# Optimization experiments

Measured on AMD Instinct MI355X. Metric: run time of the kernel, lower is better.

Reference implementation:

```python
import jax, jax.numpy as jnp
import numpy as np

N_NODES = 100000
N_EDGES = 1600000
D_IN = 128
D_HID = 128
D_OUT = 64
N_LAYERS = 3
BN_EPS = 1e-5


def _mlp_block(h, W1, b1, g, be, W2, b2):
    # PyG MLP([c_in, h, h]): Linear -> BatchNorm -> ReLU -> Linear (plain last)
    h = h @ W1 + b1                      # [N, h]
    mu = jnp.mean(h, axis=0)
    var = jnp.var(h, axis=0)             # biased var, BN training-mode stats
    h = (h - mu) * jax.lax.rsqrt(var + BN_EPS) * g + be
    h = jax.nn.relu(h)
    return h @ W2 + b2


def setup_inputs() -> dict:
    key = jax.random.key(0)
    ks = jax.random.split(key, 16)
    s_in = 1.0 / np.sqrt(D_IN)
    s_h = 1.0 / np.sqrt(D_HID)
    x = jax.random.normal(ks[0], (N_NODES, D_IN), dtype=jnp.float32)
    edge_index = jax.random.randint(ks[1], (2, N_EDGES), 0, N_NODES, dtype=jnp.int64)
    return {
        "x": x,
        "edge_index": edge_index,
        # stacked per-conv MLP params (all layers are 128->128->128)
        "W1": jax.random.normal(ks[2], (N_LAYERS, D_IN, D_HID), jnp.float32) * s_in,
        "b1": jnp.zeros((N_LAYERS, D_HID), jnp.float32),
        "g1": jnp.ones((N_LAYERS, D_HID), jnp.float32),
        "be1": jnp.zeros((N_LAYERS, D_HID), jnp.float32),
        "W2": jax.random.normal(ks[3], (N_LAYERS, D_HID, D_HID), jnp.float32) * s_h,
        "b2": jnp.zeros((N_LAYERS, D_HID), jnp.float32),
        # final MLP([h, h, out])
        "fW1": jax.random.normal(ks[4], (D_HID, D_HID), jnp.float32) * s_h,
        "fb1": jnp.zeros((D_HID,), jnp.float32),
        "fg1": jnp.ones((D_HID,), jnp.float32),
        "fbe1": jnp.zeros((D_HID,), jnp.float32),
        "fW2": jax.random.normal(ks[5], (D_HID, D_OUT), jnp.float32) * s_h,
        "fb2": jnp.zeros((D_OUT,), jnp.float32),
    }


def reference(x, edge_index, W1, b1, g1, be1, W2, b2, fW1, fb1, fg1, fbe1, fW2, fb2):
    src, dst = edge_index[0], edge_index[1]
    for l in range(N_LAYERS):
        # GINConv, eps=0: nn((1+eps)*x + sum_{j->i} x_j)
        aggr = jax.ops.segment_sum(x[src], dst, num_segments=N_NODES)  # [N, d]
        h = x + aggr
        x = jax.nn.relu(_mlp_block(h, W1[l], b1[l], g1[l], be1[l], W2[l], b2[l]))
    # final MLP (dropout=0.5 is identity in eval mode)
    return _mlp_block(x, fW1, fb1, fg1, fbe1, fW2, fb2)
```

## Files before the change

### kernel.cpp

```cpp
#include <hip/hip_runtime.h>

#define NN 100000
#define NE 1600000
#define DD 128
#define CAP 64
#define NGROUP 256

static __device__ __forceinline__ unsigned short f2b(float f) {
  unsigned int x = __float_as_uint(f);
  unsigned int r = x + 0x7fffu + ((x >> 16) & 1u);
  return (unsigned short)(r >> 16);
}
static __device__ __forceinline__ float b2f(unsigned short u) {
  return __uint_as_float(((unsigned int)u) << 16);
}

typedef __attribute__((ext_vector_type(8))) short short8;
typedef __attribute__((ext_vector_type(4))) float f32x4;

union V8 {
  uint4 u4;
  short8 s8;
  unsigned short us[8];
};

__global__ void detect_k(const int* __restrict__ ei, int* __restrict__ flag) {
  int v = ei[2 * threadIdx.x + 1];
  unsigned long long b = __ballot(v != 0);
  if (threadIdx.x == 0) *flag = (b == 0ull) ? 1 : 0;
}

__global__ __launch_bounds__(256) void cast_k(const float* __restrict__ x,
                                              unsigned short* __restrict__ x16) {
  size_t i = ((size_t)blockIdx.x * 256 + threadIdx.x) * 8;
  f32x4 a = *(const f32x4*)(x + i);
  f32x4 b = *(const f32x4*)(x + i + 4);
  V8 v;
#pragma unroll
  for (int j = 0; j < 4; ++j) {
    v.us[j] = f2b(a[j]);
    v.us[4 + j] = f2b(b[j]);
  }
  *(uint4*)(x16 + i) = v.u4;
}

__global__ __launch_bounds__(256) void pack_k(const int* __restrict__ ei,
                                              int* __restrict__ packed,
                                              int* __restrict__ cnt,
                                              const int* __restrict__ flag) {
  const int mode = *flag;
  const int gid = blockIdx.x * 256 + threadIdx.x;
  int s, d;
  if (mode) {
    s = ei[2 * (size_t)gid];
    d = ei[2 * ((size_t)NE + gid)];
  } else {
    s = ei[gid];
    d = ei[NE + gid];
  }
  packed[2 * gid] = s;
  packed[2 * gid + 1] = d;
  if (gid < NN) cnt[gid] = 0;
}

__global__ __launch_bounds__(256) void scatter_k(const long long* __restrict__ packed,
                                                 int* __restrict__ cnt,
                                                 int* __restrict__ csr) {
  const int r = blockIdx.x & 7;
  const int g = blockIdx.x >> 3;
  const int lo = r * (NN / 8), hi = lo + (NN / 8);
  for (int e = g * 256 + threadIdx.x; e < NE; e += NGROUP * 256) {
    long long sd = __builtin_nontemporal_load(&packed[e]);
    const int s = (int)(sd & 0xffffffffll);
    const int d = (int)(sd >> 32);
    if (d >= lo && d < hi) {
      int c = atomicAdd(&cnt[d], 1);
      if (c < CAP) csr[(size_t)d * CAP + c] = s;
    }
  }
}

__global__ __launch_bounds__(256) void wprep_k(const float* __restrict__ W1,
                                               const float* __restrict__ W2,
                                               const float* __restrict__ fW1,
                                               const float* __restrict__ fW2,
                                               unsigned short* __restrict__ wt) {
  int b = blockIdx.x;
  const float* src;
  int moff, N;
  if (b < 192) {
    int m = b >> 6;
    src = W1 + m * 16384;
    moff = m * 16384;
    N = 128;
    b &= 63;
  } else if (b < 384) {
    int m = (b - 192) >> 6;
    src = W2 + m * 16384;
    moff = (3 + m) * 16384;
    N = 128;
    b = (b - 192) & 63;
  } else if (b < 448) {
    src = fW1;
    moff = 6 * 16384;
    N = 128;
    b -= 384;
  } else {
    src = fW2;
    moff = 7 * 16384;
    N = 64;
    b -= 448;
  }
  int idx = b * 256 + threadIdx.x;
  int n = idx >> 7, k = idx & 127;
  if (n < N) wt[moff + idx] = f2b(src[(size_t)k * N + n]);
}

template <int AMODE, int NCOLS, int EPI, int STATS>
__global__ __launch_bounds__(256) void gemm_k(const unsigned short* __restrict__ Aptr,
                                              const unsigned short* __restrict__ wT,
                                              const float* __restrict__ bias,
                                              const float* __restrict__ bn_stats,
                                              const float* __restrict__ gamma,
                                              const float* __restrict__ beta,
                                              void* __restrict__ Cptr,
                                              float* __restrict__ stats_out,
                                              const int* __restrict__ cnt,
                                              const int* __restrict__ csr) {
  __shared__ unsigned short bT[NCOLS][136];
  __shared__ float biasS[NCOLS];
  __shared__ float scS[128];
  __shared__ float shS[128];
  __shared__ float sS[NCOLS];
  __shared__ float s2S[NCOLS];
  const int tid = threadIdx.x;

  for (int i = tid; i < NCOLS * 16; i += 256) {
    int n = i >> 4, k8 = (i & 15) << 3;
    *(uint4*)&bT[n][k8] = *(const uint4*)(wT + n * 128 + k8);
  }
  if (tid < NCOLS) biasS[tid] = bias[tid];
  if (AMODE == 2 && tid < 128) {
    const float inv_n = 1.0f / (float)NN;
    float mu = bn_stats[tid] * inv_n;
    float var = bn_stats[128 + tid] * inv_n - mu * mu;
    float sc = gamma[tid] * rsqrtf(var + 1e-5f);
    scS[tid] = sc;
    shS[tid] = beta[tid] - mu * sc;
  }
  if (STATS && tid < NCOLS) {
    sS[tid] = 0.f;
    s2S[tid] = 0.f;
  }
  __syncthreads();

  const int wv = tid >> 6;
  const int lane = tid & 63;
  const int l16 = lane & 15;
  const int quad = lane >> 4;
  const int arow = blockIdx.x * 64 + wv * 16 + l16;
  const bool rv = arow < NN;

  V8 afs[4];
  if (AMODE == 3) {
    float ac[4][8];
#pragma unroll
    for (int kc = 0; kc < 4; ++kc) {
      V8 w;
      w.u4 = rv ? *(const uint4*)(Aptr + (size_t)arow * DD + kc * 32 + quad * 8)
                : make_uint4(0u, 0u, 0u, 0u);
#pragma unroll
      for (int j = 0; j < 8; ++j) ac[kc][j] = b2f(w.us[j]);
    }
    if (rv) {
      const size_t base = (size_t)arow * CAP;
      const int c = cnt[arow];
      int p = 0;
      for (; p + 2 <= c; p += 2) {
        const int s0 = csr[base + p], s1 = csr[base + p + 1];
        V8 w0[4], w1[4];
#pragma unroll
        for (int kc = 0; kc < 4; ++kc) {
          w0[kc].u4 = *(const uint4*)(Aptr + (size_t)s0 * DD + kc * 32 + quad * 8);
          w1[kc].u4 = *(const uint4*)(Aptr + (size_t)s1 * DD + kc * 32 + quad * 8);
        }
#pragma unroll
        for (int kc = 0; kc < 4; ++kc)
#pragma unroll
          for (int j = 0; j < 8; ++j)
            ac[kc][j] += b2f(w0[kc].us[j]) + b2f(w1[kc].us[j]);
      }
      if (p < c) {
        const int s0 = csr[base + p];
        V8 w0[4];
#pragma unroll
        for (int kc = 0; kc < 4; ++kc)
          w0[kc].u4 = *(const uint4*)(Aptr + (size_t)s0 * DD + kc * 32 + quad * 8);
#pragma unroll
        for (int kc = 0; kc < 4; ++kc)
#pragma unroll
          for (int j = 0; j < 8; ++j) ac[kc][j] += b2f(w0[kc].us[j]);
      }
    }
#pragma unroll
    for (int kc = 0; kc < 4; ++kc)
#pragma unroll
      for (int j = 0; j < 8; ++j) afs[kc].us[j] = f2b(ac[kc][j]);
  } else {
#pragma unroll
    for (int kc = 0; kc < 4; ++kc) {
      const int k0 = kc * 32 + quad * 8;
      afs[kc].u4 = rv ? *(const uint4*)(Aptr + (size_t)arow * DD + k0)
                      : make_uint4(0u, 0u, 0u, 0u);
      if (AMODE == 2) {
#pragma unroll
        for (int j = 0; j < 8; ++j) {
          float f = fmaf(b2f(afs[kc].us[j]), scS[k0 + j], shS[k0 + j]);
          afs[kc].us[j] = f2b(fmaxf(f, 0.0f));
        }
      }
    }
  }

  f32x4 acc[NCOLS / 16];
#pragma unroll
  for (int nt = 0; nt < NCOLS / 16; ++nt) acc[nt] = (f32x4)(0.0f);
#pragma unroll
  for (int kc = 0; kc < 4; ++kc) {
    const int k0 = kc * 32 + quad * 8;
#pragma unroll
    for (int nt = 0; nt < NCOLS / 16; ++nt) {
      V8 bf;
      bf.u4 = *(const uint4*)&bT[nt * 16 + l16][k0];
      acc[nt] = __builtin_amdgcn_mfma_f32_16x16x32_bf16(afs[kc].s8, bf.s8, acc[nt], 0, 0, 0);
    }
  }

  const int r0 = blockIdx.x * 64 + wv * 16 + quad * 4;
#pragma unroll
  for (int nt = 0; nt < NCOLS / 16; ++nt) {
    const int col = nt * 16 + l16;
    const float bv = biasS[col];
    float s = 0.f, s2 = 0.f;
#pragma unroll
    for (int i = 0; i < 4; ++i) {
      const int r = r0 + i;
      if (r < NN) {
        float v = acc[nt][i] + bv;
        if (EPI == 1) v = fmaxf(v, 0.0f);
        if (EPI == 2) {
          ((float*)Cptr)[(size_t)r * NCOLS + col] = v;
        } else {
          unsigned short us = f2b(v);
          ((unsigned short*)Cptr)[(size_t)r * NCOLS + col] = us;
          if (STATS) {
            float vr = b2f(us);
            s += vr;
            s2 += vr * vr;
          }
        }
      }
    }
    if (STATS) {
      s += __shfl_xor(s, 16);
      s += __shfl_xor(s, 32);
      s2 += __shfl_xor(s2, 16);
      s2 += __shfl_xor(s2, 32);
      if (quad == 0) {
        atomicAdd(&sS[col], s);
        atomicAdd(&s2S[col], s2);
      }
    }
  }
  if (STATS) {
    __syncthreads();
    if (tid < NCOLS) {
      atomicAdd(&stats_out[tid], sS[tid]);
      atomicAdd(&stats_out[128 + tid], s2S[tid]);
    }
  }
}

extern "C" void kernel_launch(void* const* d_in, const int* in_sizes, int n_in,
                              void* d_out, int out_size, void* d_ws, size_t ws_size,
                              hipStream_t stream) {
  const float* x = (const float*)d_in[0];
  const int* ei = (const int*)d_in[1];
  const float* W1 = (const float*)d_in[2];
  const float* b1 = (const float*)d_in[3];
  const float* g1 = (const float*)d_in[4];
  const float* be1 = (const float*)d_in[5];
  const float* W2 = (const float*)d_in[6];
  const float* b2 = (const float*)d_in[7];
  const float* fW1 = (const float*)d_in[8];
  const float* fb1 = (const float*)d_in[9];
  const float* fg1 = (const float*)d_in[10];
  const float* fbe1 = (const float*)d_in[11];
  const float* fW2 = (const float*)d_in[12];
  const float* fb2 = (const float*)d_in[13];

  char* ws = (char*)d_ws;
  unsigned short* x16 = (unsigned short*)ws;
  unsigned short* t16 = (unsigned short*)(ws + (size_t)25600000);
  int* packed = (int*)t16;
  int* csr = (int*)(ws + (size_t)51200000);
  int* cnt = (int*)(ws + (size_t)76800000);
  float* stats4 = (float*)(ws + (size_t)77200000);
  int* flag = (int*)(ws + (size_t)77204992);
  unsigned short* wt = (unsigned short*)(ws + (size_t)77210000);

  const int vecBlocks = (NN * DD) / (256 * 8);
  const int gemmBlocks = (NN + 63) / 64;
  const int edgeBlocks = NE / 256;
  const int filtBlocks = NGROUP * 8;

  detect_k<<<1, 64, 0, stream>>>(ei, flag);
  (void)hipMemsetAsync(stats4, 0, 4 * 256 * sizeof(float), stream);
  cast_k<<<vecBlocks, 256, 0, stream>>>(x, x16);
  pack_k<<<edgeBlocks, 256, 0, stream>>>(ei, packed, cnt, flag);
  wprep_k<<<480, 256, 0, stream>>>(W1, W2, fW1, fW2, wt);
  scatter_k<<<filtBlocks, 256, 0, stream>>>((const long long*)packed, cnt, csr);

  for (int l = 0; l < 3; ++l) {
    gemm_k<3, 128, 0, 1><<<gemmBlocks, 256, 0, stream>>>(
        x16, wt + (size_t)l * 16384, b1 + l * 128, nullptr, nullptr, nullptr, t16,
        stats4 + l * 256, cnt, csr);
    gemm_k<2, 128, 1, 0><<<gemmBlocks, 256, 0, stream>>>(
        t16, wt + (size_t)(3 + l) * 16384, b2 + l * 128, stats4 + l * 256,
        g1 + l * 128, be1 + l * 128, x16, nullptr, nullptr, nullptr);
  }

  gemm_k<1, 128, 0, 1><<<gemmBlocks, 256, 0, stream>>>(
      x16, wt + (size_t)6 * 16384, fb1, nullptr, nullptr, nullptr, t16,
      stats4 + 3 * 256, nullptr, nullptr);
  gemm_k<2, 64, 2, 0><<<gemmBlocks, 256, 0, stream>>>(
      t16, wt + (size_t)7 * 16384, fb2, stats4 + 3 * 256, fg1, fbe1, (float*)d_out,
      nullptr, nullptr, nullptr);
}
```

Before: 665.9 us.

## Split aggregation into column-chunked kernel with degree-sorted node order

Result: slower. 1.341 ms (+101.4%).

```diff
diff --git a/kernel.cpp b/kernel.cpp
--- a/kernel.cpp
+++ b/kernel.cpp
@@ -17,9 +17,11 @@
 
 typedef __attribute__((ext_vector_type(8))) short short8;
 typedef __attribute__((ext_vector_type(4))) float f32x4;
+typedef unsigned int v4u __attribute__((ext_vector_type(4)));
 
 union V8 {
   uint4 u4;
+  v4u v4;
   short8 s8;
   unsigned short us[8];
 };
@@ -31,17 +33,22 @@
 }
 
 __global__ __launch_bounds__(256) void cast_k(const float* __restrict__ x,
-                                              unsigned short* __restrict__ x16) {
-  size_t i = ((size_t)blockIdx.x * 256 + threadIdx.x) * 8;
-  f32x4 a = *(const f32x4*)(x + i);
-  f32x4 b = *(const f32x4*)(x + i + 4);
-  V8 v;
+                                              unsigned short* __restrict__ xc) {
+  const int g = blockIdx.y;
+  const int n = blockIdx.x * 256 + threadIdx.x;
+  if (n >= NN) return;
+  const float* xp = x + (size_t)n * DD + g * 16;
+  V8 o0, o1;
 #pragma unroll
   for (int j = 0; j < 4; ++j) {
-    v.us[j] = f2b(a[j]);
-    v.us[4 + j] = f2b(b[j]);
-  }
-  *(uint4*)(x16 + i) = v.u4;
+    o0.us[j] = f2b(xp[j]);
+    o0.us[4 + j] = f2b(xp[4 + j]);
+    o1.us[j] = f2b(xp[8 + j]);
+    o1.us[4 + j] = f2b(xp[12 + j]);
+  }
+  unsigned short* op = xc + ((size_t)g * NN + n) * 16;
+  *(uint4*)op = o0.u4;
+  *(uint4*)(op + 8) = o1.u4;
 }
 
 __global__ __launch_bounds__(256) void pack_k(const int* __restrict__ ei,
@@ -77,6 +84,38 @@
       int c = atomicAdd(&cnt[d], 1);
       if (c < CAP) csr[(size_t)d * CAP + c] = s;
     }
+  }
+}
+
+__global__ __launch_bounds__(256) void hist2_k(const int* __restrict__ cnt,
+                                               int* __restrict__ dbin) {
+  __shared__ int lb[CAP + 1];
+  if (threadIdx.x <= CAP) lb[threadIdx.x] = 0;
+  __syncthreads();
+  const int i = blockIdx.x * 256 + threadIdx.x;
+  if (i < NN) atomicAdd(&lb[min(cnt[i], CAP)], 1);
+  __syncthreads();
+  if (threadIdx.x <= CAP && lb[threadIdx.x]) atomicAdd(&dbin[threadIdx.x], lb[threadIdx.x]);
+}
+
+__global__ void dscan_k(const int* __restrict__ dbin, int* __restrict__ dcur) {
+  if (threadIdx.x == 0) {
+    int run = 0;
+    for (int i = 0; i <= CAP; ++i) {
+      dcur[i] = run;
+      run += dbin[i];
+    }
+  }
+}
+
+__global__ __launch_bounds__(256) void dorder_k(const int* __restrict__ cnt,
+                                                int* __restrict__ dcur,
+                                                int* __restrict__ order) {
+  const int i = blockIdx.x * 256 + threadIdx.x;
+  if (i < NN) {
+    int c = min(cnt[i], CAP);
+    int pos = atomicAdd(&dcur[c], 1);
+    order[pos] = i | (c << 24);
   }
 }
 
@@ -116,6 +155,64 @@
   if (n < N) wt[moff + idx] = f2b(src[(size_t)k * N + n]);
 }
 
+__global__ __launch_bounds__(256) void agg_k(const int* __restrict__ order,
+                                             const int* __restrict__ csr,
+                                             const unsigned short* __restrict__ xc,
+                                             unsigned short* __restrict__ hc) {
+  const int g = blockIdx.x & 7;
+  const unsigned short* xg = xc + (size_t)g * NN * 16;
+  unsigned short* hg = hc + (size_t)g * NN * 16;
+  const int stride = (gridDim.x >> 3) * 256;
+  for (int i = (blockIdx.x >> 3) * 256 + threadIdx.x; i < NN; i += stride) {
+    const int oc = order[i];
+    const int n = oc & 0xFFFFFF;
+    const int c = oc >> 24;
+    V8 v0, v1;
+    v0.u4 = *(const uint4*)(xg + (size_t)n * 16);
+    v1.u4 = *(const uint4*)(xg + (size_t)n * 16 + 8);
+    float acc[16];
+#pragma unroll
+    for (int j = 0; j < 8; ++j) {
+      acc[j] = b2f(v0.us[j]);
+      acc[8 + j] = b2f(v1.us[j]);
+    }
+    const int* row = csr + (size_t)n * CAP;
+    int p = 0;
+    for (; p + 2 <= c; p += 2) {
+      const int s0 = row[p], s1 = row[p + 1];
+      V8 a0, a1, b0, b1;
+      a0.u4 = *(const uint4*)(xg + (size_t)s0 * 16);
+      a1.u4 = *(const uint4*)(xg + (size_t)s0 * 16 + 8);
+      b0.u4 = *(const uint4*)(xg + (size_t)s1 * 16);
+      b1.u4 = *(const uint4*)(xg + (size_t)s1 * 16 + 8);
+#pragma unroll
+      for (int j = 0; j < 8; ++j) {
+        acc[j] += b2f(a0.us[j]) + b2f(b0.us[j]);
+        acc[8 + j] += b2f(a1.us[j]) + b2f(b1.us[j]);
+      }
+    }
+    if (p < c) {
+      const int s0 = row[p];
+      V8 a0, a1;
+      a0.u4 = *(const uint4*)(xg + (size_t)s0 * 16);
+      a1.u4 = *(const uint4*)(xg + (size_t)s0 * 16 + 8);
+#pragma unroll
+      for (int j = 0; j < 8; ++j) {
+        acc[j] += b2f(a0.us[j]);
+        acc[8 + j] += b2f(a1.us[j]);
+      }
+    }
+    V8 o0, o1;
+#pragma unroll
+    for (int j = 0; j < 8; ++j) {
+      o0.us[j] = f2b(acc[j]);
+      o1.us[j] = f2b(acc[8 + j]);
+    }
+    __builtin_nontemporal_store(o0.v4, (v4u*)(hg + (size_t)n * 16));
+    __builtin_nontemporal_store(o1.v4, (v4u*)(hg + (size_t)n * 16 + 8));
+  }
+}
+
 template <int AMODE, int NCOLS, int EPI, int STATS>
 __global__ __launch_bounds__(256) void gemm_k(const unsigned short* __restrict__ Aptr,
                                               const unsigned short* __restrict__ wT,
@@ -124,9 +221,7 @@
                                               const float* __restrict__ gamma,
                                               const float* __restrict__ beta,
                                               void* __restrict__ Cptr,
-                                              float* __restrict__ stats_out,
-                                              const int* __restrict__ cnt,
-                                              const int* __restrict__ csr) {
+                                              float* __restrict__ stats_out) {
   __shared__ unsigned short bT[NCOLS][136];
   __shared__ float biasS[NCOLS];
   __shared__ float scS[128];
@@ -162,62 +257,21 @@
   const bool rv = arow < NN;
 
   V8 afs[4];
-  if (AMODE == 3) {
-    float ac[4][8];
-#pragma unroll
-    for (int kc = 0; kc < 4; ++kc) {
-      V8 w;
-      w.u4 = rv ? *(const uint4*)(Aptr + (size_t)arow * DD + kc * 32 + quad * 8)
-                : make_uint4(0u, 0u, 0u, 0u);
-#pragma unroll
-      for (int j = 0; j < 8; ++j) ac[kc][j] = b2f(w.us[j]);
-    }
-    if (rv) {
-      const size_t base = (size_t)arow * CAP;
-      const int c = cnt[arow];
-      int p = 0;
-      for (; p + 2 <= c; p += 2) {
-        const int s0 = csr[base + p], s1 = csr[base + p + 1];
-        V8 w0[4], w1[4];
-#pragma unroll
-        for (int kc = 0; kc < 4; ++kc) {
-          w0[kc].u4 = *(const uint4*)(Aptr + (size_t)s0 * DD + kc * 32 + quad * 8);
-          w1[kc].u4 = *(const uint4*)(Aptr + (size_t)s1 * DD + kc * 32 + quad * 8);
-        }
-#pragma unroll
-        for (int kc = 0; kc < 4; ++kc)
-#pragma unroll
-          for (int j = 0; j < 8; ++j)
-            ac[kc][j] += b2f(w0[kc].us[j]) + b2f(w1[kc].us[j]);
-      }
-      if (p < c) {
-        const int s0 = csr[base + p];
-        V8 w0[4];
-#pragma unroll
-        for (int kc = 0; kc < 4; ++kc)
-          w0[kc].u4 = *(const uint4*)(Aptr + (size_t)s0 * DD + kc * 32 + quad * 8);
-#pragma unroll
-        for (int kc = 0; kc < 4; ++kc)
-#pragma unroll
-          for (int j = 0; j < 8; ++j) ac[kc][j] += b2f(w0[kc].us[j]);
-      }
-    }
-#pragma unroll
-    for (int kc = 0; kc < 4; ++kc)
-#pragma unroll
-      for (int j = 0; j < 8; ++j) afs[kc].us[j] = f2b(ac[kc][j]);
-  } else {
-#pragma unroll
-    for (int kc = 0; kc < 4; ++kc) {
+#pragma unroll
+  for (int kc = 0; kc < 4; ++kc) {
+    if (AMODE == 1) {
+      const int col8 = kc * 4 + quad;
+      const unsigned short* ap =
+          Aptr + ((size_t)(col8 >> 1) * NN + arow) * 16 + (col8 & 1) * 8;
+      afs[kc].u4 = rv ? *(const uint4*)ap : make_uint4(0u, 0u, 0u, 0u);
+    } else {
       const int k0 = kc * 32 + quad * 8;
       afs[kc].u4 = rv ? *(const uint4*)(Aptr + (size_t)arow * DD + k0)
                       : make_uint4(0u, 0u, 0u, 0u);
-      if (AMODE == 2) {
-#pragma unroll
-        for (int j = 0; j < 8; ++j) {
-          float f = fmaf(b2f(afs[kc].us[j]), scS[k0 + j], shS[k0 + j]);
-          afs[kc].us[j] = f2b(fmaxf(f, 0.0f));
-        }
+#pragma unroll
+      for (int j = 0; j < 8; ++j) {
+        float f = fmaf(b2f(afs[kc].us[j]), scS[k0 + j], shS[k0 + j]);
+        afs[kc].us[j] = f2b(fmaxf(f, 0.0f));
       }
     }
   }
@@ -247,9 +301,11 @@
       const int r = r0 + i;
       if (r < NN) {
         float v = acc[nt][i] + bv;
-        if (EPI == 1) v = fmaxf(v, 0.0f);
         if (EPI == 2) {
           ((float*)Cptr)[(size_t)r * NCOLS + col] = v;
+        } else if (EPI == 3) {
+          v = fmaxf(v, 0.0f);
+          ((unsigned short*)Cptr)[((size_t)nt * NN + r) * 16 + l16] = f2b(v);
         } else {
           unsigned short us = f2b(v);
           ((unsigned short*)Cptr)[(size_t)r * NCOLS + col] = us;
@@ -300,40 +356,49 @@
   const float* fb2 = (const float*)d_in[13];
 
   char* ws = (char*)d_ws;
-  unsigned short* x16 = (unsigned short*)ws;
+  unsigned short* xc = (unsigned short*)ws;
   unsigned short* t16 = (unsigned short*)(ws + (size_t)25600000);
   int* packed = (int*)t16;
   int* csr = (int*)(ws + (size_t)51200000);
   int* cnt = (int*)(ws + (size_t)76800000);
-  float* stats4 = (float*)(ws + (size_t)77200000);
-  int* flag = (int*)(ws + (size_t)77204992);
-  unsigned short* wt = (unsigned short*)(ws + (size_t)77210000);
-
-  const int vecBlocks = (NN * DD) / (256 * 8);
+  int* order = (int*)(ws + (size_t)77200000);
+  char* smallz = ws + (size_t)77600000;
+  int* dbin = (int*)smallz;
+  int* dcur = (int*)(smallz + 1024);
+  float* stats4 = (float*)(smallz + 2048);
+  int* flag = (int*)(ws + (size_t)77608192);
+  unsigned short* wt = (unsigned short*)(ws + (size_t)77610240);
+  unsigned short* hc = (unsigned short*)d_out;
+
   const int gemmBlocks = (NN + 63) / 64;
   const int edgeBlocks = NE / 256;
+  const int nodeBlocks = (NN + 255) / 256;
   const int filtBlocks = NGROUP * 8;
 
   detect_k<<<1, 64, 0, stream>>>(ei, flag);
-  (void)hipMemsetAsync(stats4, 0, 4 * 256 * sizeof(float), stream);
-  cast_k<<<vecBlocks, 256, 0, stream>>>(x, x16);
+  (void)hipMemsetAsync(smallz, 0, 8192, stream);
+  cast_k<<<dim3(nodeBlocks, 8), 256, 0, stream>>>(x, xc);
   pack_k<<<edgeBlocks, 256, 0, stream>>>(ei, packed, cnt, flag);
   wprep_k<<<480, 256, 0, stream>>>(W1, W2, fW1, fW2, wt);
   scatter_k<<<filtBlocks, 256, 0, stream>>>((const long long*)packed, cnt, csr);
+  hist2_k<<<nodeBlocks, 256, 0, stream>>>(cnt, dbin);
+  dscan_k<<<1, 64, 0, stream>>>(dbin, dcur);
+  dorder_k<<<nodeBlocks, 256, 0, stream>>>(cnt, dcur, order);
 
   for (int l = 0; l < 3; ++l) {
-    gemm_k<3, 128, 0, 1><<<gemmBlocks, 256, 0, stream>>>(
-        x16, wt + (size_t)l * 16384, b1 + l * 128, nullptr, nullptr, nullptr, t16,
-        stats4 + l * 256, cnt, csr);
-    gemm_k<2, 128, 1, 0><<<gemmBlocks, 256, 0, stream>>>(
+    agg_k<<<1024, 256, 0, stream>>>(order, csr, xc, hc);
+    gemm_k<1, 128, 0, 1><<<gemmBlocks, 256, 0, stream>>>(
+        hc, wt + (size_t)l * 16384, b1 + l * 128, nullptr, nullptr, nullptr, t16,
+        stats4 + l * 256);
+    gemm_k<2, 128, 3, 0><<<gemmBlocks, 256, 0, stream>>>(
         t16, wt + (size_t)(3 + l) * 16384, b2 + l * 128, stats4 + l * 256,
-        g1 + l * 128, be1 + l * 128, x16, nullptr, nullptr, nullptr);
+        g1 + l * 128, be1 + l * 128, xc, nullptr);
   }
 
   gemm_k<1, 128, 0, 1><<<gemmBlocks, 256, 0, stream>>>(
-      x16, wt + (size_t)6 * 16384, fb1, nullptr, nullptr, nullptr, t16,
-      stats4 + 3 * 256, nullptr, nullptr);
+      xc, wt + (size_t)6 * 16384, fb1, nullptr, nullptr, nullptr, t16,
+      stats4 + 3 * 256);
   gemm_k<2, 64, 2, 0><<<gemmBlocks, 256, 0, stream>>>(
       t16, wt + (size_t)7 * 16384, fb2, stats4 + 3 * 256, fg1, fbe1, (float*)d_out,
-      nullptr, nullptr, nullptr);
-}
+      nullptr);
+}
```
